# Performance work log

Measured on AMD Instinct MI355X. Metric: run time of the kernel, lower is better.

Reference implementation:

```python
import jax, jax.numpy as jnp
from jax import lax
import numpy as np

B, NUM_WS, Z_DIM, MAT_DIM = 2048, 16, 512, 10
MIDDLE, OUT_DIM, N_POST = 512, 512, 4


def setup_inputs() -> dict:
    key = jax.random.key(0)
    ks = jax.random.split(key, 16)
    inp = {
        "z": jax.random.normal(ks[0], (B, NUM_WS, Z_DIM), dtype=jnp.float32),
        # init_alg_basis_multi: normal with std = lie_alg_init_scale = 0.001
        "lie_alg_basis": jax.random.normal(ks[1], (NUM_WS, Z_DIM, MAT_DIM, MAT_DIM), dtype=jnp.float32) * 0.001,
    }
    in_f = MAT_DIM * MAT_DIM
    for i in range(N_POST + 1):
        out_f = OUT_DIM if i == N_POST else MIDDLE
        fan_in = in_f * 3
        inp[f"W{i}"] = jax.random.normal(ks[2 + i], (out_f, in_f, 3), dtype=jnp.float32) / np.sqrt(fan_in)
        inp[f"b{i}"] = jnp.zeros((out_f,), dtype=jnp.float32)
        in_f = out_f
    return inp


def _conv1d(x, W, b):
    # x: [b, C_in, L], W: [C_out, C_in, 3] -> [b, C_out, L], stride 1, pad 1
    y = lax.conv_general_dilated(x, W, window_strides=(1,), padding="SAME",
                                 dimension_numbers=("NCH", "OIH", "NCH"))
    return y + b[None, :, None]


def reference(z, lie_alg_basis, W0, b0, W1, b1, W2, b2, W3, b3, W4, b4):
    b, num_ws, z_dim = z.shape
    m = lie_alg_basis.shape[-1]
    # lie algebra combination: sum_z z[b,w,z] * basis[w,z,i,j]
    lie_alg = jnp.einsum("bwz,wzij->bwij", z, lie_alg_basis)  # [b, num_ws, m, m]
    # batched small matrix exponential
    lie_group = jax.vmap(jax.scipy.linalg.expm)(lie_alg.reshape(b * num_ws, m, m))
    gfeat = lie_group.reshape(b, num_ws, m * m)
    # conv1d decoder over the num_ws axis
    x = gfeat.transpose(0, 2, 1)  # [b, m*m, num_ws]
    for W, bb in ((W0, b0), (W1, b1), (W2, b2), (W3, b3)):
        x = jax.nn.relu(_conv1d(x, W, bb))
    x = _conv1d(x, W4, b4)
    return x.transpose(0, 2, 1)  # [b, num_ws, out_dim]
```

## Files before the change

### kernel.cpp

```cpp
#include <hip/hip_runtime.h>


typedef __attribute__((ext_vector_type(8))) short short8;
typedef __attribute__((ext_vector_type(4))) float f32x4;

#define NWS 16
#define ZD 512
#define MM 100

static __device__ __forceinline__ unsigned short f2bf(float f) {
    union { float f; unsigned u; } x; x.f = f;
    unsigned r = x.u + 0x7fffu + ((x.u >> 16) & 1u);
    return (unsigned short)(r >> 16);
}
static __device__ __forceinline__ float bf2f(unsigned short b) {
    union { unsigned u; float f; } x; x.u = ((unsigned)b) << 16; return x.f;
}

__global__ __launch_bounds__(256) void lie_gemm(const float* __restrict__ Z,
                                                const float* __restrict__ Basis,
                                                float* __restrict__ Out) {
    __shared__ float As[16][132];
    __shared__ float Bs[16][128];
    const int w = blockIdx.y;
    const int row0 = blockIdx.x * 128;
    const int tid = threadIdx.x;
    const int tx = tid & 15, ty = tid >> 4;
    float acc[8][8];
#pragma unroll
    for (int r = 0; r < 8; ++r)
#pragma unroll
        for (int c = 0; c < 8; ++c) acc[r][c] = 0.f;

    for (int k0 = 0; k0 < ZD; k0 += 16) {
#pragma unroll
        for (int ii = 0; ii < 8; ++ii) {
            int u = tid * 8 + ii;
            int kk = u & 15, m = u >> 4;
            As[kk][m] = Z[(size_t)((row0 + m) * NWS + w) * ZD + (k0 + kk)];
        }
#pragma unroll
        for (int ii = 0; ii < 8; ++ii) {
            int u = tid + ii * 256;
            int n = u & 127, kk = u >> 7;
            Bs[kk][n] = (n < MM) ? Basis[(size_t)(w * ZD + k0 + kk) * MM + n] : 0.f;
        }
        __syncthreads();
#pragma unroll
        for (int kk = 0; kk < 16; ++kk) {
            float a[8], b[8];
#pragma unroll
            for (int r = 0; r < 8; ++r) a[r] = As[kk][ty * 8 + r];
#pragma unroll
            for (int c = 0; c < 8; ++c) b[c] = Bs[kk][tx * 8 + c];
#pragma unroll
            for (int r = 0; r < 8; ++r)
#pragma unroll
                for (int c = 0; c < 8; ++c) acc[r][c] += a[r] * b[c];
        }
        __syncthreads();
    }
#pragma unroll
    for (int r = 0; r < 8; ++r) {
        int b = row0 + ty * 8 + r;
#pragma unroll
        for (int c = 0; c < 8; ++c) {
            int col = tx * 8 + c;
            if (col < MM) Out[(size_t)(b * NWS + w) * MM + col] = acc[r][c];
        }
    }
}

__global__ __launch_bounds__(256) void expm_kernel(const float* __restrict__ Ain,
                                                   unsigned short* __restrict__ Ghi,
                                                   unsigned short* __restrict__ Glo) {
    __shared__ float Pm[16][104];
    __shared__ float Am[16][104];
    const int tid = threadIdx.x;
    const int q = tid >> 7;
    const int e = tid & 127;
    const bool act = (e < MM);
    const int ee = act ? e : 0;
    const int i = ee / 10;
    const int j = ee - i * 10;
    const int base = blockIdx.x * 16;

    float a[8], p[8], s[8];
    float colA[8][10];

#pragma unroll
    for (int m = 0; m < 8; ++m) {
        int mat = base + q * 8 + m;
        a[m] = act ? Ain[(size_t)mat * MM + e] : 0.f;
        if (act) Am[q * 8 + m][e] = a[m];
    }
    __syncthreads();
#pragma unroll
    for (int m = 0; m < 8; ++m)
#pragma unroll
        for (int k = 0; k < 10; ++k) colA[m][k] = Am[q * 8 + m][k * 10 + j];

#pragma unroll
    for (int m = 0; m < 8; ++m) {
        p[m] = a[m];
        s[m] = a[m] + ((i == j) ? 1.f : 0.f);
    }

#pragma unroll
    for (int t = 2; t <= 14; ++t) {
        __syncthreads();
#pragma unroll
        for (int m = 0; m < 8; ++m)
            if (act) Pm[q * 8 + m][e] = p[m];
        __syncthreads();
        const float inv = 1.f / (float)t;
#pragma unroll
        for (int m = 0; m < 8; ++m) {
            float np = 0.f;
#pragma unroll
            for (int k = 0; k < 10; ++k) np += Pm[q * 8 + m][i * 10 + k] * colA[m][k];
            p[m] = np * inv;
            s[m] += p[m];
        }
    }
#pragma unroll
    for (int m = 0; m < 8; ++m) {
        size_t off = (size_t)(base + q * 8 + m) * 128 + e;
        float v = act ? s[m] : 0.f;
        unsigned short h = f2bf(v);
        Ghi[off] = h;
        Glo[off] = f2bf(v - bf2f(h));
    }
}

template <int CIN_REAL, int CINP>
__global__ void wtrans_bf(const float* __restrict__ W,
                          unsigned short* __restrict__ Whi,
                          unsigned short* __restrict__ Wlo) {
    int idx = blockIdx.x * 256 + threadIdx.x;
    if (idx >= 512 * 3 * CINP) return;
    int co = idx / (3 * CINP);
    int k = idx - co * (3 * CINP);
    int t = k / CINP, ci = k - t * CINP;
    float v = (ci < CIN_REAL) ? W[(size_t)(co * CIN_REAL + ci) * 3 + t] : 0.f;
    unsigned short h = f2bf(v);
    Whi[idx] = h;
    Wlo[idx] = f2bf(v - bf2f(h));
}

template <int RELU, int CINP, int PAIR_OUT>
__global__ __launch_bounds__(256) void conv_mfma(
    const unsigned short* __restrict__ Xhi, const unsigned short* __restrict__ Xlo,
    const unsigned short* __restrict__ Whi, const unsigned short* __restrict__ Wlo,
    const float* __restrict__ Bias,
    unsigned short* __restrict__ Yhi, unsigned short* __restrict__ Ylo,
    float* __restrict__ Yf) {
    __shared__ __align__(16) unsigned short AH[128 * 32];
    __shared__ __align__(16) unsigned short AL[128 * 32];
    __shared__ __align__(16) unsigned short BH[128 * 32];
    __shared__ __align__(16) unsigned short BL[128 * 32];
    const int tid = threadIdx.x;
    const int lane = tid & 63;
    const int wv = tid >> 6;
    const int wr = (wv >> 1) * 64;
    const int wc = (wv & 1) * 64;
    const int row0 = blockIdx.x * 128;
    const int col0 = blockIdx.y * 128;

    f32x4 acc[4][4] = {};

    for (int t = 0; t < 3; ++t) {
        for (int c = 0; c < CINP; c += 32) {
            __syncthreads();
#pragma unroll
            for (int rep = 0; rep < 2; ++rep) {
                int u = tid + rep * 256;
                int m = u >> 2, g = u & 3;
                int ldso = m * 32 + ((g ^ ((m >> 1) & 3)) << 3);
                int sl = (m & 15) + t - 1;
                short8 vh = {}, vl = {};
                if (sl >= 0 && sl < 16) {
                    size_t ga = (size_t)(row0 + m + t - 1) * CINP + c + g * 8;
                    vh = *(const short8*)&Xhi[ga];
                    vl = *(const short8*)&Xlo[ga];
                }
                *(short8*)&AH[ldso] = vh;
                *(short8*)&AL[ldso] = vl;
                size_t ba = (size_t)(col0 + m) * (3 * CINP) + t * CINP + c + g * 8;
                *(short8*)&BH[ldso] = *(const short8*)&Whi[ba];
                *(short8*)&BL[ldso] = *(const short8*)&Wlo[ba];
            }
            __syncthreads();
            short8 ah[4], al[4], bh[4], bl[4];
#pragma unroll
            for (int mt = 0; mt < 4; ++mt) {
                int m = wr + mt * 16 + (lane & 15);
                int off = m * 32 + ((((lane >> 4) ^ ((m >> 1) & 3))) << 3);
                ah[mt] = *(const short8*)&AH[off];
                al[mt] = *(const short8*)&AL[off];
            }
#pragma unroll
            for (int nt = 0; nt < 4; ++nt) {
                int n = wc + nt * 16 + (lane & 15);
                int off = n * 32 + ((((lane >> 4) ^ ((n >> 1) & 3))) << 3);
                bh[nt] = *(const short8*)&BH[off];
                bl[nt] = *(const short8*)&BL[off];
            }
#pragma unroll
            for (int mt = 0; mt < 4; ++mt)
#pragma unroll
                for (int nt = 0; nt < 4; ++nt) {
                    acc[mt][nt] = __builtin_amdgcn_mfma_f32_16x16x32_bf16(ah[mt], bl[nt], acc[mt][nt], 0, 0, 0);
                    acc[mt][nt] = __builtin_amdgcn_mfma_f32_16x16x32_bf16(al[mt], bh[nt], acc[mt][nt], 0, 0, 0);
                    acc[mt][nt] = __builtin_amdgcn_mfma_f32_16x16x32_bf16(ah[mt], bh[nt], acc[mt][nt], 0, 0, 0);
                }
        }
    }
    float bcol[4];
#pragma unroll
    for (int nt = 0; nt < 4; ++nt) bcol[nt] = Bias[col0 + wc + nt * 16 + (lane & 15)];
#pragma unroll
    for (int mt = 0; mt < 4; ++mt)
#pragma unroll
        for (int nt = 0; nt < 4; ++nt) {
            int gcol = col0 + wc + nt * 16 + (lane & 15);
#pragma unroll
            for (int i = 0; i < 4; ++i) {
                int grow = row0 + wr + mt * 16 + 4 * (lane >> 4) + i;
                float v = acc[mt][nt][i] + bcol[nt];
                if (RELU) v = fmaxf(v, 0.f);
                size_t off = (size_t)grow * 512 + gcol;
                if (PAIR_OUT) {
                    unsigned short h = f2bf(v);
                    Yhi[off] = h;
                    Ylo[off] = f2bf(v - bf2f(h));
                } else {
                    Yf[off] = v;
                }
            }
        }
}

extern "C" void kernel_launch(void* const* d_in, const int* in_sizes, int n_in,
                              void* d_out, int out_size, void* d_ws, size_t ws_size,
                              hipStream_t stream) {
    (void)in_sizes; (void)n_in; (void)out_size; (void)ws_size;
    const float* z     = (const float*)d_in[0];
    const float* basis = (const float*)d_in[1];
    const float* W0 = (const float*)d_in[2];  const float* b0 = (const float*)d_in[3];
    const float* W1 = (const float*)d_in[4];  const float* b1 = (const float*)d_in[5];
    const float* W2 = (const float*)d_in[6];  const float* b2 = (const float*)d_in[7];
    const float* W3 = (const float*)d_in[8];  const float* b3 = (const float*)d_in[9];
    const float* W4 = (const float*)d_in[10]; const float* b4 = (const float*)d_in[11];
    float* out = (float*)d_out;
    char* ws = (char*)d_ws;
    const size_t MB = 1ull << 20;

    float* lieA = out;
    unsigned short* Ghi = (unsigned short*)(ws);
    unsigned short* Glo = (unsigned short*)(ws + 8 * MB);
    unsigned short* PAhi = (unsigned short*)((char*)d_out);
    unsigned short* PAlo = (unsigned short*)((char*)d_out + 32 * MB);
    unsigned short* PBhi = (unsigned short*)(ws);
    unsigned short* PBlo = (unsigned short*)(ws + 32 * MB);
    unsigned short* Wnhi = (unsigned short*)(ws + 64 * MB);
    unsigned short* Wnlo = (unsigned short*)(ws + 64 * MB + 1572864);

    lie_gemm<<<dim3(16, 16), 256, 0, stream>>>(z, basis, lieA);
    expm_kernel<<<2048, 256, 0, stream>>>(lieA, Ghi, Glo);

    wtrans_bf<100, 128><<<768, 256, 0, stream>>>(W0, Wnhi, Wnlo);
    conv_mfma<1, 128, 1><<<dim3(256, 4), 256, 0, stream>>>(Ghi, Glo, Wnhi, Wnlo, b0, PAhi, PAlo, nullptr);

    wtrans_bf<512, 512><<<3072, 256, 0, stream>>>(W1, Wnhi, Wnlo);
    conv_mfma<1, 512, 1><<<dim3(256, 4), 256, 0, stream>>>(PAhi, PAlo, Wnhi, Wnlo, b1, PBhi, PBlo, nullptr);
    wtrans_bf<512, 512><<<3072, 256, 0, stream>>>(W2, Wnhi, Wnlo);
    conv_mfma<1, 512, 1><<<dim3(256, 4), 256, 0, stream>>>(PBhi, PBlo, Wnhi, Wnlo, b2, PAhi, PAlo, nullptr);
    wtrans_bf<512, 512><<<3072, 256, 0, stream>>>(W3, Wnhi, Wnlo);
    conv_mfma<1, 512, 1><<<dim3(256, 4), 256, 0, stream>>>(PAhi, PAlo, Wnhi, Wnlo, b3, PBhi, PBlo, nullptr);

    wtrans_bf<512, 512><<<3072, 256, 0, stream>>>(W4, Wnhi, Wnlo);
    conv_mfma<0, 512, 0><<<dim3(256, 4), 256, 0, stream>>>(PBhi, PBlo, Wnhi, Wnlo, b4, nullptr, nullptr, out);
}
```

Baseline: 1.083 ms.

## Load conv tiles directly into LDS and remap blocks across XCDs

The conv MFMA kernel now fills its shared-memory tiles with global_load_lds, skipping the round trip through registers. The XOR swizzle moves to the global source address so each lane's 16 bytes land in a linear LDS slot. Padded rows are still zeroed with ordinary stores. The launch becomes a 1D grid with a block-index remap (bid&7 times 128) so consecutive row/column tiles are grouped per XCD for better L2 reuse. Mixing direct-to-LDS writes with ordinary LDS stores relies on the existing barriers for correctness.

```diff
diff --git a/kernel.cpp b/kernel.cpp
--- a/kernel.cpp
+++ b/kernel.cpp
@@ -7,6 +7,11 @@
 #define NWS 16
 #define ZD 512
 #define MM 100
+
+#define GLDS(SRC, DST)                                                        \
+    __builtin_amdgcn_global_load_lds(                                         \
+        (const __attribute__((address_space(1))) void*)(SRC),                 \
+        (__attribute__((address_space(3))) void*)(DST), 16, 0, 0)
 
 static __device__ __forceinline__ unsigned short f2bf(float f) {
     union { float f; unsigned u; } x; x.f = f;
@@ -164,8 +169,10 @@
     const int wv = tid >> 6;
     const int wr = (wv >> 1) * 64;
     const int wc = (wv & 1) * 64;
-    const int row0 = blockIdx.x * 128;
-    const int col0 = blockIdx.y * 128;
+    const int bid = blockIdx.x;
+    const int e = ((bid & 7) << 7) + (bid >> 3);
+    const int row0 = (e >> 2) * 128;
+    const int col0 = (e & 3) * 128;
 
     f32x4 acc[4][4] = {};
 
@@ -174,21 +181,26 @@
             __syncthreads();
 #pragma unroll
             for (int rep = 0; rep < 2; ++rep) {
-                int u = tid + rep * 256;
-                int m = u >> 2, g = u & 3;
-                int ldso = m * 32 + ((g ^ ((m >> 1) & 3)) << 3);
-                int sl = (m & 15) + t - 1;
-                short8 vh = {}, vl = {};
+                const int slotbase = wv * 128 + rep * 64;
+                const int slot = slotbase + lane;
+                const int m = slot >> 2;
+                const int gs = slot & 3;
+                const int gsrc = gs ^ ((m >> 1) & 3);
+                {
+                    size_t ba = (size_t)(col0 + m) * (3 * CINP) + t * CINP + c + gsrc * 8;
+                    GLDS(&Whi[ba], &BH[slotbase * 8]);
+                    GLDS(&Wlo[ba], &BL[slotbase * 8]);
+                }
+                const int sl = (m & 15) + t - 1;
                 if (sl >= 0 && sl < 16) {
-                    size_t ga = (size_t)(row0 + m + t - 1) * CINP + c + g * 8;
-                    vh = *(const short8*)&Xhi[ga];
-                    vl = *(const short8*)&Xlo[ga];
-                }
-                *(short8*)&AH[ldso] = vh;
-                *(short8*)&AL[ldso] = vl;
-                size_t ba = (size_t)(col0 + m) * (3 * CINP) + t * CINP + c + g * 8;
-                *(short8*)&BH[ldso] = *(const short8*)&Whi[ba];
-                *(short8*)&BL[ldso] = *(const short8*)&Wlo[ba];
+                    size_t ga = (size_t)(row0 + m + t - 1) * CINP + c + gsrc * 8;
+                    GLDS(&Xhi[ga], &AH[slotbase * 8]);
+                    GLDS(&Xlo[ga], &AL[slotbase * 8]);
+                } else {
+                    short8 z = {};
+                    *(short8*)&AH[slot * 8] = z;
+                    *(short8*)&AL[slot * 8] = z;
+                }
             }
             __syncthreads();
             short8 ah[4], al[4], bh[4], bl[4];
@@ -270,15 +282,15 @@
     expm_kernel<<<2048, 256, 0, stream>>>(lieA, Ghi, Glo);
 
     wtrans_bf<100, 128><<<768, 256, 0, stream>>>(W0, Wnhi, Wnlo);
-    conv_mfma<1, 128, 1><<<dim3(256, 4), 256, 0, stream>>>(Ghi, Glo, Wnhi, Wnlo, b0, PAhi, PAlo, nullptr);
+    conv_mfma<1, 128, 1><<<1024, 256, 0, stream>>>(Ghi, Glo, Wnhi, Wnlo, b0, PAhi, PAlo, nullptr);
 
     wtrans_bf<512, 512><<<3072, 256, 0, stream>>>(W1, Wnhi, Wnlo);
-    conv_mfma<1, 512, 1><<<dim3(256, 4), 256, 0, stream>>>(PAhi, PAlo, Wnhi, Wnlo, b1, PBhi, PBlo, nullptr);
+    conv_mfma<1, 512, 1><<<1024, 256, 0, stream>>>(PAhi, PAlo, Wnhi, Wnlo, b1, PBhi, PBlo, nullptr);
     wtrans_bf<512, 512><<<3072, 256, 0, stream>>>(W2, Wnhi, Wnlo);
-    conv_mfma<1, 512, 1><<<dim3(256, 4), 256, 0, stream>>>(PBhi, PBlo, Wnhi, Wnlo, b2, PAhi, PAlo, nullptr);
+    conv_mfma<1, 512, 1><<<1024, 256, 0, stream>>>(PBhi, PBlo, Wnhi, Wnlo, b2, PAhi, PAlo, nullptr);
     wtrans_bf<512, 512><<<3072, 256, 0, stream>>>(W3, Wnhi, Wnlo);
-    conv_mfma<1, 512, 1><<<dim3(256, 4), 256, 0, stream>>>(PAhi, PAlo, Wnhi, Wnlo, b3, PBhi, PBlo, nullptr);
+    conv_mfma<1, 512, 1><<<1024, 256, 0, stream>>>(PAhi, PAlo, Wnhi, Wnlo, b3, PBhi, PBlo, nullptr);
 
     wtrans_bf<512, 512><<<3072, 256, 0, stream>>>(W4, Wnhi, Wnlo);
-    conv_mfma<0, 512, 0><<<dim3(256, 4), 256, 0, stream>>>(PBhi, PBlo, Wnhi, Wnlo, b4, nullptr, nullptr, out);
-}
+    conv_mfma<0, 512, 0><<<1024, 256, 0, stream>>>(PBhi, PBlo, Wnhi, Wnlo, b4, nullptr, nullptr, out);
+}
```

Measured after the change: 969.8 us. 10.5% less time.
